# Kernel optimization log

Measured on AMD Instinct MI355X. Metric: run time of the kernel, lower is better.

The kernel has to match this reference:

```python
import jax, jax.numpy as jnp
import numpy as np

B, M, T, D, V = 16, 1024, 4096, 512, 32000
HOPS = 2  # multi_layer_gcn layer_number=2


def setup_inputs() -> dict:
    key = jax.random.key(0)
    ks = jax.random.split(key, 10)
    s = 1.0 / np.sqrt(D)
    emb = jax.random.normal(ks[0], (V, D), jnp.float32) * 0.02
    Ws = jax.random.normal(ks[1], (HOPS, D, D), jnp.float32) * s
    Wn = jax.random.normal(ks[2], (HOPS, D, D), jnp.float32) * s
    Wr = jax.random.normal(ks[3], (HOPS, D, D), jnp.float32) * s
    Wt = jax.random.normal(ks[4], (D, 3 * D), jnp.float32) * (1.0 / np.sqrt(3 * D))
    concept_ids = jax.random.randint(ks[5], (B, M), 0, V)
    relation = jax.random.randint(ks[6], (B, T), 0, V)
    head = jax.random.randint(ks[7], (B, T), 0, M)
    tail = jax.random.randint(ks[8], (B, T), 0, M)
    triple_label = jax.random.randint(ks[9], (B, T), -1, 2)  # {-1,0,1}
    return dict(emb=emb, Ws=Ws, Wn=Wn, Wr=Wr, Wt=Wt,
                concept_ids=concept_ids, relation=relation,
                head=head, tail=tail, triple_label=triple_label)


def _forward(emb, Ws, Wn, Wr, Wt, concept_ids, relation, head, tail, triple_label):
    x = emb[concept_ids]        # [B, M, D] node hidden
    rel = emb[relation]         # [B, T, D] relation hidden
    mask = (triple_label != -1).astype(x.dtype)  # [B, T]

    # per-batch scatter_add into M node slots
    scat = jax.vmap(lambda msg, idx: jnp.zeros((M, msg.shape[-1]), msg.dtype).at[idx].add(msg))
    scat1 = jax.vmap(lambda v, idx: jnp.zeros((M,), v.dtype).at[idx].add(v))

    for i in range(HOPS):
        oh = jnp.take_along_axis(x, head[..., None], axis=1) * mask[..., None]  # gather heads
        ot = jnp.take_along_axis(x, tail[..., None], axis=1) * mask[..., None]  # gather tails
        relm = rel * mask[..., None]
        # update_node += scatter(head_repr - rel -> tail) + scatter(tail_repr - rel -> head)
        upd = scat(oh - relm, tail) + scat(ot - relm, head)          # [B, M, D]
        cnt = scat1(mask, tail) + scat1(mask, head)                  # [B, M]
        x = jax.nn.relu(
            jnp.einsum('bmd,ed->bme', x, Ws[i])
            + jnp.einsum('bmd,ed->bme', upd, Wn[i]) / jnp.maximum(cnt, 1.0)[..., None]
        )
        rel = jnp.einsum('btd,ed->bte', rel, Wr[i])

    head_repr = jnp.take_along_axis(x, head[..., None], axis=1)  # [B, T, D]
    tail_repr = jnp.take_along_axis(x, tail[..., None], axis=1)  # [B, T, D]
    triple_repr = jnp.concatenate([head_repr, rel, tail_repr], axis=-1)  # [B, T, 3D]
    triple_repr = jnp.einsum('btk,dk->btd', triple_repr, Wt)     # [B, T, D]
    encoded_cause = triple_repr.sum(axis=1)                      # [B, D]
    return triple_repr, encoded_cause


def reference(emb, Ws, Wn, Wr, Wt, concept_ids, relation, head, tail, triple_label):
    return _forward(emb, Ws, Wn, Wr, Wt, concept_ids, relation, head, tail, triple_label)
```

## Files before the change

### kernel.cpp

```cpp
#include <hip/hip_runtime.h>

namespace {

constexpr int kB = 16;
constexpr int kM = 1024;
constexpr int kT = 4096;
constexpr int kD = 512;
constexpr int kV = 32000;

typedef __attribute__((ext_vector_type(8))) short bfrag8;
typedef __attribute__((ext_vector_type(4))) float f4acc;

__device__ __forceinline__ ushort f2bf(float f) {
  unsigned u = __float_as_uint(f);
  u += 0x7fffu + ((u >> 16) & 1u);
  return (ushort)(u >> 16);
}
__device__ __forceinline__ float bf2f(ushort h) {
  return __uint_as_float(((unsigned)h) << 16);
}

__device__ __forceinline__ void gload_lds16(const void* g, void* l) {
  __builtin_amdgcn_global_load_lds(
      (const __attribute__((address_space(1))) void*)g,
      (__attribute__((address_space(3))) void*)l, 16, 0, 0);
}

constexpr int kN0 = kV * kD / 4;
constexpr int kN1 = kN0 + 2 * kD * kD / 4;
constexpr int kN2 = kN1 + 2 * kD * kD / 4;
constexpr int kN3 = kN2 + kD * 1536 / 4;
constexpr int kN4 = kN3 + kB * kM * 128;
constexpr int kPREPB = kN4 / 8192;
constexpr int kCSRB = 16;
constexpr int kMM2B = 256;

__global__ __launch_bounds__(512) void fused_prep_k(
    const float4* __restrict__ emb, const float4* __restrict__ Ws,
    const float4* __restrict__ Wn, const float4* __restrict__ Wt,
    const float* __restrict__ Wnf, const float* __restrict__ Wtf,
    const float* __restrict__ Wrf,
    const int* __restrict__ cid,
    const int* __restrict__ headp, const int* __restrict__ tailp,
    const int* __restrict__ lblp,
    ushort4* __restrict__ EMBb, ushort4* __restrict__ Wsb,
    ushort4* __restrict__ Wnb, ushort4* __restrict__ Wtb,
    ushort4* __restrict__ X0,
    int* __restrict__ deg, int* __restrict__ rowstart, int* __restrict__ epack,
    ushort* __restrict__ Wn2r, float* __restrict__ T1)
{
  __shared__ __align__(16) char shm[45056];
  const int bid = blockIdx.x;
  const int tid = threadIdx.x;

  if (bid < kCSRB) {
    int* sdeg = (int*)shm;
    int* sscan = (int*)(shm + 4096);
    int* sfill = (int*)(shm + 8192);
    int* sep = (int*)(shm + 12288);
    const int b = bid;
    const int n0 = tid, n1 = tid + 512;
    sdeg[n0] = 0; sdeg[n1] = 0;
    __syncthreads();
    const int* hb = headp + (b << 12);
    const int* tb = tailp + (b << 12);
    const int* lb = lblp + (b << 12);
    for (int t = tid; t < kT; t += 512) {
      if (lb[t] == -1) continue;
      atomicAdd(&sdeg[tb[t]], 1);
      atomicAdd(&sdeg[hb[t]], 1);
    }
    __syncthreads();
    int d0 = sdeg[n0], d1 = sdeg[n1];
    sscan[n0] = d0; sscan[n1] = d1;
    __syncthreads();
    for (int off = 1; off < kM; off <<= 1) {
      int v0 = (n0 >= off) ? sscan[n0 - off] : 0;
      int v1 = (n1 >= off) ? sscan[n1 - off] : 0;
      __syncthreads();
      sscan[n0] += v0; sscan[n1] += v1;
      __syncthreads();
    }
    int lrs0 = sscan[n0] - d0;
    int lrs1 = sscan[n1] - d1;
    deg[(b << 10) + n0] = d0;
    deg[(b << 10) + n1] = d1;
    rowstart[(b << 10) + n0] = b * (2 * kT) + lrs0;
    rowstart[(b << 10) + n1] = b * (2 * kT) + lrs1;
    sfill[n0] = lrs0; sfill[n1] = lrs1;
    __syncthreads();
    for (int t = tid; t < kT; t += 512) {
      if (lb[t] == -1) continue;
      int hd = hb[t];
      int tl = tb[t];
      int p0 = atomicAdd(&sfill[tl], 1);
      sep[p0] = ((t * 2) << 10) | hd;
      int p1 = atomicAdd(&sfill[hd], 1);
      sep[p1] = ((t * 2 + 1) << 10) | tl;
    }
    __syncthreads();
#pragma unroll
    for (int nn = 0; nn < 2; ++nn) {
      int lrs = nn ? lrs1 : lrs0;
      int d = nn ? d1 : d0;
      for (int i = 1; i < d; ++i) {
        int key = sep[lrs + i];
        int j = i - 1;
        while (j >= 0 && sep[lrs + j] > key) {
          sep[lrs + j + 1] = sep[lrs + j];
          --j;
        }
        sep[lrs + j + 1] = key;
      }
    }
    __syncthreads();
    for (int i = tid; i < 2 * kT; i += 512)
      epack[b * (2 * kT) + i] = sep[i];
  } else if (bid < kCSRB + kPREPB) {
    const int bidp = bid - kCSRB;
    for (int c = 0; c < 4; ++c) {
      const int base = (bidp * 4 + c) * 2048 + tid;
      const float4* sp[4];
      ushort4* dp[4];
#pragma unroll
      for (int j = 0; j < 4; ++j) {
        int i = base + j * 512;
        if (i < kN0) { sp[j] = emb + i; dp[j] = EMBb + i; }
        else if (i < kN1) { sp[j] = Ws + (i - kN0); dp[j] = Wsb + (i - kN0); }
        else if (i < kN2) { sp[j] = Wn + (i - kN1); dp[j] = Wnb + (i - kN1); }
        else if (i < kN3) { sp[j] = Wt + (i - kN2); dp[j] = Wtb + (i - kN2); }
        else {
          int idx = i - kN3;
          sp[j] = emb + (size_t)cid[idx >> 7] * 128 + (idx & 127);
          dp[j] = X0 + idx;
        }
      }
      float4 v[4];
#pragma unroll
      for (int j = 0; j < 4; ++j) v[j] = *sp[j];
#pragma unroll
      for (int j = 0; j < 4; ++j) {
        ushort4 o;
        o.x = f2bf(v[j].x); o.y = f2bf(v[j].y);
        o.z = f2bf(v[j].z); o.w = f2bf(v[j].w);
        *dp[j] = o;
      }
    }
  } else {
    float (*prow)[512] = (float(*)[512])shm;
    const int mb = bid - kCSRB - kPREPB;
    const int job = mb >> 7;
    const int e0 = (mb & 127) * 4;
    const int k = tid;
    const float* P;
    int strideP, offsP;
    const float* Q;
    if (job == 0) { P = Wnf + (size_t)kD * kD; strideP = 512; offsP = 0; Q = Wrf; }
    else { P = Wtf; strideP = 1536; offsP = 512; Q = Wrf + (size_t)kD * kD; }
#pragma unroll
    for (int i = 0; i < 4; ++i)
      prow[i][k] = P[(size_t)(e0 + i) * strideP + offsP + k];
    __syncthreads();
    float acc[4] = {0.f, 0.f, 0.f, 0.f};
    for (int a = 0; a < 512; ++a) {
      float qv = Q[a * 512 + k];
#pragma unroll
      for (int i = 0; i < 4; ++i) acc[i] = fmaf(prow[i][a], qv, acc[i]);
    }
#pragma unroll
    for (int i = 0; i < 4; ++i) {
      if (job == 0) Wn2r[(e0 + i) * 512 + k] = f2bf(acc[i]);
      else T1[(e0 + i) * 512 + k] = acc[i];
    }
  }
}

constexpr int kFOLDB = 128;

__global__ __launch_bounds__(512) void fold_aggxr_k(
    const float* __restrict__ T1, const float* __restrict__ Wrf,
    ushort* __restrict__ Wfold,
    const ushort4* __restrict__ Xv, const ushort4* __restrict__ EMBv,
    const int* __restrict__ relid,
    const int* __restrict__ deg, const int* __restrict__ rowstart,
    const int* __restrict__ epack,
    ushort4* __restrict__ SxC, ushort4* __restrict__ nSr0n)
{
  __shared__ float prow[4][512];
  const int bid = blockIdx.x;
  const int tid = threadIdx.x;
  if (bid < kFOLDB) {
    int e0 = bid * 4;
    int k = tid;
#pragma unroll
    for (int i = 0; i < 4; ++i)
      prow[i][k] = T1[(size_t)(e0 + i) * 512 + k];
    __syncthreads();
    float acc[4] = {0.f, 0.f, 0.f, 0.f};
    for (int a = 0; a < 512; ++a) {
      float qv = Wrf[a * 512 + k];
#pragma unroll
      for (int i = 0; i < 4; ++i) acc[i] = fmaf(prow[i][a], qv, acc[i]);
    }
#pragma unroll
    for (int i = 0; i < 4; ++i) Wfold[(e0 + i) * 512 + k] = f2bf(acc[i]);
  } else {
    int bm = (bid - kFOLDB) * 4 + (tid >> 7);
    int t128 = tid & 127;
    int b = bm >> 10;
    int dg = deg[bm];
    int rs = rowstart[bm];
    const int* rid = relid + (b << 12);
    size_t xbase = (size_t)b * kM * 128;
    float ax = 0.f, ay = 0.f, az = 0.f, aw = 0.f;
    float rx = 0.f, ry = 0.f, rz = 0.f, rw = 0.f;
    int e = 0;
    for (; e + 4 <= dg; e += 4) {
      int pk[4];
#pragma unroll
      for (int j = 0; j < 4; ++j) pk[j] = epack[rs + e + j];
      ushort4 xv[4], rv[4];
#pragma unroll
      for (int j = 0; j < 4; ++j) {
        xv[j] = Xv[xbase + (size_t)(pk[j] & 1023) * 128 + t128];
        rv[j] = EMBv[(size_t)rid[pk[j] >> 11] * 128 + t128];
      }
#pragma unroll
      for (int j = 0; j < 4; ++j) {
        ax += bf2f(xv[j].x); ay += bf2f(xv[j].y);
        az += bf2f(xv[j].z); aw += bf2f(xv[j].w);
        rx += bf2f(rv[j].x); ry += bf2f(rv[j].y);
        rz += bf2f(rv[j].z); rw += bf2f(rv[j].w);
      }
    }
    for (; e < dg; ++e) {
      int pk = epack[rs + e];
      ushort4 xv = Xv[xbase + (size_t)(pk & 1023) * 128 + t128];
      ushort4 rv = EMBv[(size_t)rid[pk >> 11] * 128 + t128];
      ax += bf2f(xv.x); ay += bf2f(xv.y); az += bf2f(xv.z); aw += bf2f(xv.w);
      rx += bf2f(rv.x); ry += bf2f(rv.y); rz += bf2f(rv.z); rw += bf2f(rv.w);
    }
    float s = 1.0f / (float)(dg > 0 ? dg : 1);
    ushort4 o;
    o.x = f2bf((ax - rx) * s); o.y = f2bf((ay - ry) * s);
    o.z = f2bf((az - rz) * s); o.w = f2bf((aw - rw) * s);
    SxC[(size_t)bm * 128 + t128] = o;
    o.x = f2bf(-rx * s); o.y = f2bf(-ry * s);
    o.z = f2bf(-rz * s); o.w = f2bf(-rw * s);
    nSr0n[(size_t)bm * 128 + t128] = o;
  }
}

__global__ __launch_bounds__(128) void agg_x_k(
    const ushort4* __restrict__ Xv,
    const int* __restrict__ deg, const int* __restrict__ rowstart,
    const int* __restrict__ epack, ushort4* __restrict__ outv)
{
  int bm = blockIdx.x;
  int b = bm >> 10;
  int tid = threadIdx.x;
  int dg = deg[bm];
  int rs = rowstart[bm];
  size_t xbase = (size_t)b * kM * 128;
  float ax = 0.f, ay = 0.f, az = 0.f, aw = 0.f;
  int e = 0;
  for (; e + 4 <= dg; e += 4) {
    int pk[4];
#pragma unroll
    for (int j = 0; j < 4; ++j) pk[j] = epack[rs + e + j];
    ushort4 xv[4];
#pragma unroll
    for (int j = 0; j < 4; ++j)
      xv[j] = Xv[xbase + (size_t)(pk[j] & 1023) * 128 + tid];
#pragma unroll
    for (int j = 0; j < 4; ++j) {
      ax += bf2f(xv[j].x); ay += bf2f(xv[j].y);
      az += bf2f(xv[j].z); aw += bf2f(xv[j].w);
    }
  }
  for (; e < dg; ++e) {
    int src = epack[rs + e] & 1023;
    ushort4 xv = Xv[xbase + (size_t)src * 128 + tid];
    ax += bf2f(xv.x); ay += bf2f(xv.y); az += bf2f(xv.z); aw += bf2f(xv.w);
  }
  float s = 1.0f / (float)(dg > 0 ? dg : 1);
  ushort4 o;
  o.x = f2bf(ax * s); o.y = f2bf(ay * s); o.z = f2bf(az * s); o.w = f2bf(aw * s);
  outv[(size_t)bm * 128 + tid] = o;
}

template<int MODE>
__global__ __launch_bounds__(256) void gemm_k(
    const ushort* __restrict__ A0, const ushort* __restrict__ A1,
    const ushort* __restrict__ A2,
    const ushort* __restrict__ W1, const ushort* __restrict__ W2,
    const ushort* __restrict__ W3,
    ushort* __restrict__ outbf)
{
  constexpr int NSEG = (MODE == 0) ? 3 : (MODE == 1) ? 2 : 1;
  constexpr bool RELU = (MODE == 0) || (MODE == 1);
  constexpr int NC = (MODE == 4) ? 8 : 4;
  constexpr int OSTR = (MODE == 4) ? 1024 : 512;
  constexpr bool SWZ = (MODE != 5);

  __shared__ __align__(16) char lds[32768];
  char* ldsA = lds;
  char* ldsB = lds + 16384;
  const int tid = threadIdx.x;
  const int w = tid >> 6;
  const int l = tid & 63;
  const int wr = w >> 1;
  const int wc = w & 1;
  const int bid = blockIdx.x;
  int panel, col;
  if constexpr (SWZ) {
    int xcd = bid & 7;
    int idx = bid >> 3;
    panel = xcd * (((int)gridDim.x >> 3) / NC) + idx / NC;
    col = idx % NC;
  } else {
    panel = bid >> 2;
    col = bid & 3;
  }
  const int rowBase = panel * 128;
  const int colBase = col * 128;

  f4acc acc[4][4];
#pragma unroll
  for (int i = 0; i < 4; ++i)
#pragma unroll
    for (int j = 0; j < 4; ++j) acc[i][j] = (f4acc)(0.f);

  int lrow[4], gc[4];
#pragma unroll
  for (int i = 0; i < 4; ++i) {
    int P = (i * 4 + w) * 64 + l;
    lrow[i] = P >> 3;
    gc[i] = (P & 7) ^ (lrow[i] & 7);
  }

  for (int seg = 0; seg < NSEG; ++seg) {
    const char* aP[4];
    const char* bP[4];
#pragma unroll
    for (int i = 0; i < 4; ++i) {
      int grow = rowBase + lrow[i];
      const ushort* ab;
      if constexpr (MODE == 0) {
        ab = (seg == 0 ? A0 : (seg == 1 ? A1 : A2)) + (size_t)grow * kD;
      } else if constexpr (MODE == 1) {
        ab = (seg == 0 ? A0 : A1) + (size_t)grow * kD;
      } else {
        ab = A0 + (size_t)grow * kD;
      }
      aP[i] = (const char*)ab + gc[i] * 16;
      int e = colBase + lrow[i];
      const ushort* wb;
      if constexpr (MODE == 0) {
        wb = (seg == 0 ? W1 : (seg == 1 ? W2 : W3)) + (size_t)e * kD;
      } else if constexpr (MODE == 1) {
        wb = (seg == 0 ? W1 : W2) + (size_t)e * kD;
      } else if constexpr (MODE == 4) {
        wb = W1 + (size_t)(e & 511) * 1536 + (e >> 9) * 1024;
      } else {
        wb = W1 + (size_t)e * kD;
      }
      bP[i] = (const char*)wb + gc[i] * 16;
    }
    for (int kcl = 0; kcl < 8; ++kcl) {
      __syncthreads();
#pragma unroll
      for (int i = 0; i < 4; ++i) {
        gload_lds16(aP[i] + kcl * 128, ldsA + (i * 4 + w) * 1024);
        gload_lds16(bP[i] + kcl * 128, ldsB + (i * 4 + w) * 1024);
      }
      __syncthreads();
#pragma unroll
      for (int ksub = 0; ksub < 2; ++ksub) {
        bfrag8 ef[4], wf[4];
#pragma unroll
        for (int mi = 0; mi < 4; ++mi) {
          int r = wr * 64 + mi * 16 + (l & 15);
          int g = (ksub * 4 + (l >> 4)) ^ (r & 7);
          ef[mi] = *(const bfrag8*)(ldsA + r * 128 + g * 16);
        }
#pragma unroll
        for (int ni = 0; ni < 4; ++ni) {
          int e = wc * 64 + ni * 16 + (l & 15);
          int g = (ksub * 4 + (l >> 4)) ^ (e & 7);
          wf[ni] = *(const bfrag8*)(ldsB + e * 128 + g * 16);
        }
#pragma unroll
        for (int mi = 0; mi < 4; ++mi)
#pragma unroll
          for (int ni = 0; ni < 4; ++ni)
            acc[mi][ni] = __builtin_amdgcn_mfma_f32_16x16x32_bf16(
                wf[ni], ef[mi], acc[mi][ni], 0, 0, 0);
      }
    }
  }

#pragma unroll
  for (int mi = 0; mi < 4; ++mi) {
    int rr = rowBase + wr * 64 + mi * 16 + (l & 15);
#pragma unroll
    for (int ni = 0; ni < 4; ++ni) {
      int cc0 = colBase + wc * 64 + ni * 16 + (l >> 4) * 4;
      float v0 = acc[mi][ni][0], v1 = acc[mi][ni][1];
      float v2 = acc[mi][ni][2], v3 = acc[mi][ni][3];
      if constexpr (RELU) {
        v0 = fmaxf(v0, 0.f); v1 = fmaxf(v1, 0.f);
        v2 = fmaxf(v2, 0.f); v3 = fmaxf(v3, 0.f);
      }
      ushort4 o;
      o.x = f2bf(v0); o.y = f2bf(v1); o.z = f2bf(v2); o.w = f2bf(v3);
      *(ushort4*)(outbf + (size_t)rr * OSTR + cc0) = o;
    }
  }
}

__global__ __launch_bounds__(128) void final_add_k(
    const ushort4* __restrict__ REL2v, const ushort4* __restrict__ HTv,
    const int* __restrict__ relid, const int* __restrict__ headp,
    const int* __restrict__ tailp,
    float* __restrict__ outf, float* __restrict__ part)
{
  const int blk = blockIdx.x;
  const int tid = threadIdx.x;
  const int r0 = blk * 32;
  float cs0 = 0.f, cs1 = 0.f, cs2 = 0.f, cs3 = 0.f;
  for (int i = 0; i < 32; i += 8) {
    ushort4 rv[8], hv[8], tv[8];
#pragma unroll
    for (int j = 0; j < 8; ++j) {
      int r = r0 + i + j;
      int bb = r >> 12;
      rv[j] = REL2v[(size_t)relid[r] * 128 + tid];
      hv[j] = HTv[((size_t)(bb << 10) + headp[r]) * 256 + tid];
      tv[j] = HTv[((size_t)(bb << 10) + tailp[r]) * 256 + 128 + tid];
    }
#pragma unroll
    for (int j = 0; j < 8; ++j) {
      f4acc ov;
      ov[0] = bf2f(rv[j].x) + bf2f(hv[j].x) + bf2f(tv[j].x);
      ov[1] = bf2f(rv[j].y) + bf2f(hv[j].y) + bf2f(tv[j].y);
      ov[2] = bf2f(rv[j].z) + bf2f(hv[j].z) + bf2f(tv[j].z);
      ov[3] = bf2f(rv[j].w) + bf2f(hv[j].w) + bf2f(tv[j].w);
      cs0 += ov[0]; cs1 += ov[1]; cs2 += ov[2]; cs3 += ov[3];
      __builtin_nontemporal_store(
          ov, (f4acc*)(outf + (size_t)(r0 + i + j) * 512 + tid * 4));
    }
  }
  float4 o; o.x = cs0; o.y = cs1; o.z = cs2; o.w = cs3;
  *(float4*)(part + (size_t)blk * 512 + tid * 4) = o;
}

__global__ __launch_bounds__(512) void reduce_enc_k(
    const float* __restrict__ part, float* __restrict__ enc)
{
  int b = blockIdx.x;
  int c = threadIdx.x;
  float s = 0.f;
  for (int rt = 0; rt < 128; ++rt) s += part[(size_t)(b * 128 + rt) * 512 + c];
  enc[b * 512 + c] = s;
}

}

extern "C" void kernel_launch(void* const* d_in, const int* in_sizes, int n_in,
                              void* d_out, int out_size, void* d_ws, size_t ws_size,
                              hipStream_t stream) {
  const float* emb = (const float*)d_in[0];
  const float* Ws = (const float*)d_in[1];
  const float* Wn = (const float*)d_in[2];
  const float* Wr = (const float*)d_in[3];
  const float* Wt = (const float*)d_in[4];
  const int* cid = (const int*)d_in[5];
  const int* relid = (const int*)d_in[6];
  const int* headp = (const int*)d_in[7];
  const int* tailp = (const int*)d_in[8];
  const int* lblp = (const int*)d_in[9];
  float* out = (float*)d_out;

  char* wsp = (char*)d_ws;
  ushort* EMBb  = (ushort*)(wsp);
  ushort* HT    = (ushort*)(wsp);
  ushort* REL2  = (ushort*)(wsp + (32ull << 20));
  ushort* Wsb   = (ushort*)(wsp + (64ull << 20));
  ushort* Wnb   = (ushort*)(wsp + (65ull << 20));
  ushort* Wtb   = (ushort*)(wsp + (66ull << 20));
  ushort* Wn2r  = (ushort*)(wsp + (67ull << 20) + (512ull << 10));
  ushort* Wfold = (ushort*)(wsp + (68ull << 20));
  float*  T1    = (float*)(wsp + (68ull << 20) + (512ull << 10));
  int* deg      = (int*)(wsp + (70ull << 20));
  int* rowstart = deg + kB * kM;
  int* epack    = rowstart + kB * kM;
  float* part   = (float*)(wsp + (71ull << 20));

  char* outc = (char*)d_out;
  ushort* X0    = (ushort*)(outc);
  ushort* Sxn   = (ushort*)(outc + (16ull << 20));
  ushort* nSr0n = (ushort*)(outc + (32ull << 20));
  ushort* X1    = (ushort*)(outc + (48ull << 20));
  ushort* X2    = X0;
  float* ENC = out + (size_t)kB * kT * kD;

  fused_prep_k<<<kCSRB + kPREPB + kMM2B, 512, 0, stream>>>(
      (const float4*)emb, (const float4*)Ws, (const float4*)Wn,
      (const float4*)Wt, Wn, Wt, Wr, cid, headp, tailp, lblp,
      (ushort4*)EMBb, (ushort4*)Wsb, (ushort4*)Wnb, (ushort4*)Wtb,
      (ushort4*)X0, deg, rowstart, epack, Wn2r, T1);

  fold_aggxr_k<<<kFOLDB + kB * kM / 4, 512, 0, stream>>>(
      T1, Wr, Wfold, (const ushort4*)X0, (const ushort4*)EMBb, relid,
      deg, rowstart, epack, (ushort4*)Sxn, (ushort4*)nSr0n);

  gemm_k<1><<<(kB * kM / 128) * 4, 256, 0, stream>>>(
      X0, Sxn, nullptr, Wsb, Wnb, nullptr, X1);

  gemm_k<5><<<(kV / 128) * 4, 256, 0, stream>>>(
      EMBb, nullptr, nullptr, Wfold, nullptr, nullptr, REL2);

  agg_x_k<<<kB * kM, 128, 0, stream>>>(
      (const ushort4*)X1, deg, rowstart, epack, (ushort4*)Sxn);

  gemm_k<0><<<(kB * kM / 128) * 4, 256, 0, stream>>>(
      X1, Sxn, nSr0n, Wsb + (size_t)kD * kD, Wnb + (size_t)kD * kD, Wn2r, X2);

  gemm_k<4><<<(kB * kM / 128) * 8, 256, 0, stream>>>(
      X2, nullptr, nullptr, Wtb, nullptr, nullptr, HT);

  final_add_k<<<kB * kT / 32, 128, 0, stream>>>(
      (const ushort4*)REL2, (const ushort4*)HT, relid, headp, tailp, out, part);

  reduce_enc_k<<<kB, 512, 0, stream>>>(part, ENC);
}
```

Baseline: 263.0 us.

## Build CSR edge lists with an LDS bitonic sort instead of atomic fill

CSR construction now writes a packed (node, sequence) key for every edge slot in shared memory, with masked edges set to a max sentinel. A full bitonic sort of 8192 keys then replaces the atomic scatter-fill and the per-row insertion sort. This removes the per-node atomics and the load-imbalanced serial sorts, and it frees some shared memory. In exchange it adds about ninety barrier-separated sort stages in each of the 16 CSR blocks, and it re-reads head and tail from global memory to rebuild the packed entries.

```diff
diff --git a/kernel.cpp b/kernel.cpp
--- a/kernel.cpp
+++ b/kernel.cpp
@@ -49,15 +49,14 @@
     int* __restrict__ deg, int* __restrict__ rowstart, int* __restrict__ epack,
     ushort* __restrict__ Wn2r, float* __restrict__ T1)
 {
-  __shared__ __align__(16) char shm[45056];
+  __shared__ __align__(16) char shm[40960];
   const int bid = blockIdx.x;
   const int tid = threadIdx.x;
 
   if (bid < kCSRB) {
     int* sdeg = (int*)shm;
     int* sscan = (int*)(shm + 4096);
-    int* sfill = (int*)(shm + 8192);
-    int* sep = (int*)(shm + 12288);
+    unsigned* keys = (unsigned*)(shm + 8192);
     const int b = bid;
     const int n0 = tid, n1 = tid + 512;
     sdeg[n0] = 0; sdeg[n1] = 0;
@@ -66,9 +65,17 @@
     const int* tb = tailp + (b << 12);
     const int* lb = lblp + (b << 12);
     for (int t = tid; t < kT; t += 512) {
-      if (lb[t] == -1) continue;
-      atomicAdd(&sdeg[tb[t]], 1);
-      atomicAdd(&sdeg[hb[t]], 1);
+      bool m = (lb[t] != -1);
+      int hd = hb[t];
+      int tl = tb[t];
+      if (m) {
+        atomicAdd(&sdeg[tl], 1);
+        atomicAdd(&sdeg[hd], 1);
+      }
+      keys[2 * t]     = m ? (((unsigned)tl << 13) | (unsigned)(2 * t))
+                          : 0xFFFFFFFFu;
+      keys[2 * t + 1] = m ? (((unsigned)hd << 13) | (unsigned)(2 * t + 1))
+                          : 0xFFFFFFFFu;
     }
     __syncthreads();
     int d0 = sdeg[n0], d1 = sdeg[n1];
@@ -81,41 +88,30 @@
       sscan[n0] += v0; sscan[n1] += v1;
       __syncthreads();
     }
-    int lrs0 = sscan[n0] - d0;
-    int lrs1 = sscan[n1] - d1;
     deg[(b << 10) + n0] = d0;
     deg[(b << 10) + n1] = d1;
-    rowstart[(b << 10) + n0] = b * (2 * kT) + lrs0;
-    rowstart[(b << 10) + n1] = b * (2 * kT) + lrs1;
-    sfill[n0] = lrs0; sfill[n1] = lrs1;
+    rowstart[(b << 10) + n0] = b * (2 * kT) + sscan[n0] - d0;
+    rowstart[(b << 10) + n1] = b * (2 * kT) + sscan[n1] - d1;
+    for (int k = 2; k <= 8192; k <<= 1) {
+      for (int j = k >> 1; j > 0; j >>= 1) {
+        __syncthreads();
+        for (int i = tid; i < 8192; i += 512) {
+          int p = i ^ j;
+          if (p > i) {
+            unsigned a = keys[i], c = keys[p];
+            bool up = ((i & k) == 0);
+            if ((a > c) == up) { keys[i] = c; keys[p] = a; }
+          }
+        }
+      }
+    }
     __syncthreads();
-    for (int t = tid; t < kT; t += 512) {
-      if (lb[t] == -1) continue;
-      int hd = hb[t];
-      int tl = tb[t];
-      int p0 = atomicAdd(&sfill[tl], 1);
-      sep[p0] = ((t * 2) << 10) | hd;
-      int p1 = atomicAdd(&sfill[hd], 1);
-      sep[p1] = ((t * 2 + 1) << 10) | tl;
-    }
-    __syncthreads();
-#pragma unroll
-    for (int nn = 0; nn < 2; ++nn) {
-      int lrs = nn ? lrs1 : lrs0;
-      int d = nn ? d1 : d0;
-      for (int i = 1; i < d; ++i) {
-        int key = sep[lrs + i];
-        int j = i - 1;
-        while (j >= 0 && sep[lrs + j] > key) {
-          sep[lrs + j + 1] = sep[lrs + j];
-          --j;
-        }
-        sep[lrs + j + 1] = key;
-      }
-    }
-    __syncthreads();
-    for (int i = tid; i < 2 * kT; i += 512)
-      epack[b * (2 * kT) + i] = sep[i];
+    for (int i = tid; i < 2 * kT; i += 512) {
+      int seq = (int)(keys[i] & 8191u);
+      int t = seq >> 1;
+      int src = (seq & 1) ? tb[t] : hb[t];
+      epack[b * (2 * kT) + i] = (seq << 10) | src;
+    }
   } else if (bid < kCSRB + kPREPB) {
     const int bidp = bid - kCSRB;
     for (int c = 0; c < 4; ++c) {
```

After: 387.3 us. 1.47x slower.
